# Performance work log

Measured on AMD Instinct MI355X. Metric: run time of the kernel, lower is better.

The kernel has to match this reference:

```python
import jax, jax.numpy as jnp
import numpy as np

N, E, F_IN = 50000, 800000, 64
H, C1, C2 = 4, 32, 64
NUM_GRAPHS, NUM_CLASSES = 128, 8
NEG_SLOPE = 0.2


def _glorot(key, shape):
    fan_in, fan_out = shape[1], shape[0]
    lim = (6.0 / (fan_in + fan_out)) ** 0.5
    return jax.random.uniform(key, shape, jnp.float32, -lim, lim)


def setup_inputs() -> dict:
    key = jax.random.key(0)
    ks = jax.random.split(key, 20)
    x = jax.random.normal(ks[0], (N, F_IN), jnp.float32)
    edge_index = jax.random.randint(ks[1], (2, E), 0, N, jnp.int64)
    batch = jnp.sort(jax.random.randint(ks[2], (N,), 0, NUM_GRAPHS, jnp.int64))
    d1, d2 = H * C1, H * C2
    return {
        "x": x, "edge_index": edge_index, "batch": batch,
        # GATv2 layer 1 (F_IN -> 32, 4 heads)
        "Wl1": _glorot(ks[3], (d1, F_IN)), "bl1": jnp.zeros((d1,), jnp.float32),
        "Wr1": _glorot(ks[4], (d1, F_IN)), "br1": jnp.zeros((d1,), jnp.float32),
        "att1": _glorot(ks[5], (H, C1)), "bias1": jnp.zeros((d1,), jnp.float32),
        # GATv2 layer 2 (128 -> 64, 4 heads)
        "Wl2": _glorot(ks[6], (d2, d1)), "bl2": jnp.zeros((d2,), jnp.float32),
        "Wr2": _glorot(ks[7], (d2, d1)), "br2": jnp.zeros((d2,), jnp.float32),
        "att2": _glorot(ks[8], (H, C2)), "bias2": jnp.zeros((d2,), jnp.float32),
        # classifier: Linear(256,128) -> ReLU -> (Dropout eval=id) -> Linear(128,8)
        "Wf1": _glorot(ks[9], (128, d2)), "bf1": jnp.zeros((128,), jnp.float32),
        "Wf2": _glorot(ks[10], (NUM_CLASSES, 128)), "bf2": jnp.zeros((NUM_CLASSES,), jnp.float32),
    }


def _gatv2(x, src, dst, Wl, bl, Wr, br, att, bias, heads, out_ch):
    # PyG GATv2Conv: xl = lin_l(x) (source), xr = lin_r(x) (target)
    xl = (x @ Wl.T + bl).reshape(N, heads, out_ch)
    xr = (x @ Wr.T + br).reshape(N, heads, out_ch)
    # per-edge score: att . LeakyReLU(xl[j] + xr[i])  -> [E', H]
    e = jnp.sum(jax.nn.leaky_relu(xl[src] + xr[dst], NEG_SLOPE) * att, axis=-1)
    # destination-grouped softmax (self-loops guarantee every node has an edge)
    emax = jax.ops.segment_max(e, dst, num_segments=N)
    ex = jnp.exp(e - emax[dst])
    denom = jax.ops.segment_sum(ex, dst, num_segments=N)
    alpha = ex / denom[dst]  # [E', H]
    out = jax.ops.segment_sum(alpha[:, :, None] * xl[src], dst, num_segments=N)
    return out.reshape(N, heads * out_ch) + bias


def reference(x, edge_index, batch, Wl1, bl1, Wr1, br1, att1, bias1,
              Wl2, bl2, Wr2, br2, att2, bias2, Wf1, bf1, Wf2, bf2):
    # add self loops (PyG default add_self_loops=True)
    loops = jnp.arange(N, dtype=edge_index.dtype)
    src = jnp.concatenate([edge_index[0], loops])
    dst = jnp.concatenate([edge_index[1], loops])
    h = jax.nn.elu(_gatv2(x, src, dst, Wl1, bl1, Wr1, br1, att1, bias1, H, C1))
    h = jax.nn.elu(_gatv2(h, src, dst, Wl2, bl2, Wr2, br2, att2, bias2, H, C2))
    # global mean pool over graphs
    sums = jax.ops.segment_sum(h, batch, num_segments=NUM_GRAPHS)
    cnts = jax.ops.segment_sum(jnp.ones((N,), h.dtype), batch, num_segments=NUM_GRAPHS)
    pooled = sums / jnp.maximum(cnts, 1.0)[:, None]  # [G, 256]
    # classifier (dropout inactive at inference)
    z = jax.nn.relu(pooled @ Wf1.T + bf1)
    return z @ Wf2.T + bf2
```

## Files before the change

kernel.cpp:

```cpp
#include <hip/hip_runtime.h>
#include <hip/hip_bf16.h>
#include <math.h>

#define NN 50000
#define NE 800000
#define NEP (NE + NN)
#define NG 128
#define PSPLIT 16
#define NSB ((NN + 255) / 256)

typedef unsigned short u16;
typedef __bf16 bf16x8 __attribute__((ext_vector_type(8)));
typedef float f32x4 __attribute__((ext_vector_type(4)));

#define L2E 1.4426950408889634f

__device__ __forceinline__ float eluf(float v) {
  return v > 0.0f ? v : expm1f(v);
}
__device__ __forceinline__ float bflo(unsigned u) {
  union { unsigned i; float f; } c; c.i = u << 16; return c.f;
}
__device__ __forceinline__ float bfhi(unsigned u) {
  union { unsigned i; float f; } c; c.i = u & 0xffff0000u; return c.f;
}
__device__ __forceinline__ bf16x8 load8(const u16* p) {
  union { uint4 u; bf16x8 v; } c;
  c.u = *(const uint4*)p;
  return c.v;
}

__global__ __launch_bounds__(256) void k_deg(const int* __restrict__ ei, int* __restrict__ deg) {
  int t = blockIdx.x * 256 + threadIdx.x;
  if (t >= NEP) return;
  int dst = (t < NE) ? ei[NE + t] : (t - NE);
  atomicAdd(&deg[dst], 1);
}

__global__ __launch_bounds__(256) void k_scan1(const int* __restrict__ deg, int* __restrict__ bsum) {
  __shared__ int red[256];
  int i = blockIdx.x * 256 + threadIdx.x;
  red[threadIdx.x] = (i < NN) ? deg[i] : 0;
  __syncthreads();
  for (int off = 128; off > 0; off >>= 1) {
    if (threadIdx.x < off) red[threadIdx.x] += red[threadIdx.x + off];
    __syncthreads();
  }
  if (threadIdx.x == 0) bsum[blockIdx.x] = red[0];
}

__global__ __launch_bounds__(256) void k_scan2(int* __restrict__ bsum) {
  __shared__ int s[256];
  int t = threadIdx.x;
  s[t] = (t < NSB) ? bsum[t] : 0;
  __syncthreads();
  for (int off = 1; off < 256; off <<= 1) {
    int v = (t >= off) ? s[t - off] : 0;
    __syncthreads();
    s[t] += v;
    __syncthreads();
  }
  if (t < NSB) bsum[t] = (t == 0) ? 0 : s[t - 1];
}

__global__ __launch_bounds__(256) void k_scan3(const int* __restrict__ deg, const int* __restrict__ bsum,
                                               int* __restrict__ rowptr) {
  __shared__ int s[256];
  int t = threadIdx.x;
  int i = blockIdx.x * 256 + t;
  s[t] = (i < NN) ? deg[i] : 0;
  __syncthreads();
  for (int off = 1; off < 256; off <<= 1) {
    int v = (t >= off) ? s[t - off] : 0;
    __syncthreads();
    s[t] += v;
    __syncthreads();
  }
  int excl = (t == 0) ? 0 : s[t - 1];
  if (i <= NN) rowptr[i] = bsum[blockIdx.x] + excl;
}

__global__ __launch_bounds__(256) void k_scatter(const int* __restrict__ ei, const int* __restrict__ rowptr,
                                                 int* __restrict__ fill, int* __restrict__ srcidx) {
  int t = blockIdx.x * 256 + threadIdx.x;
  if (t >= NEP) return;
  int src, dst;
  if (t < NE) { src = ei[t]; dst = ei[NE + t]; } else { src = t - NE; dst = src; }
  int pos = atomicAdd(&fill[dst], 1);
  srcidx[rowptr[dst] + pos] = src;
}

__global__ __launch_bounds__(256) void k_cvtx(const float* __restrict__ x, u16* __restrict__ o, int n4) {
  int t = blockIdx.x * 256 + threadIdx.x;
  if (t >= n4) return;
  float4 v = ((const float4*)x)[t];
  __hip_bfloat16 b[4] = {__float2bfloat16(v.x), __float2bfloat16(v.y),
                         __float2bfloat16(v.z), __float2bfloat16(v.w)};
  ((uint2*)o)[t] = *(uint2*)b;
}

__global__ __launch_bounds__(256) void k_cvtw(const float* __restrict__ w1, const float* __restrict__ w2,
                                              const float* __restrict__ w3, const float* __restrict__ w4,
                                              u16* __restrict__ o) {
  int t = blockIdx.x * 256 + threadIdx.x;
  if (t >= 81920) return;
  float v;
  if (t < 8192) v = w1[t];
  else if (t < 16384) v = w2[t - 8192];
  else if (t < 49152) v = w3[t - 16384];
  else v = w4[t - 49152];
  __hip_bfloat16 b = __float2bfloat16(v);
  o[t] = *(u16*)&b;
}

template <int K>
__global__ __launch_bounds__(256) void k_mfma(const u16* __restrict__ Xb,
                                              const u16* __restrict__ Wlb, const u16* __restrict__ Wrb,
                                              const float* __restrict__ bl, const float* __restrict__ br,
                                              __hip_bfloat16* __restrict__ Yl, float* __restrict__ Yr,
                                              int dout) {
  int lane = threadIdx.x & 63;
  int wid = threadIdx.x >> 6;
  int r0 = blockIdx.x * 64 + wid * 16;
  int c0 = blockIdx.y * 64;
  bool isR = (blockIdx.z != 0);
  const u16* W = isR ? Wrb : Wlb;
  const float* bias = isR ? br : bl;

  int arow = min(r0 + (lane & 15), NN - 1);
  int koff = (lane >> 4) * 8;
  const u16* ap = Xb + (size_t)arow * K + koff;
  const u16* bp = W + (size_t)(c0 + (lane & 15)) * K + koff;

  f32x4 acc[4] = {};
#pragma unroll
  for (int ks = 0; ks < K / 32; ++ks) {
    bf16x8 a  = load8(ap + ks * 32);
    bf16x8 b0 = load8(bp + ks * 32);
    bf16x8 b1 = load8(bp + 16 * K + ks * 32);
    bf16x8 b2 = load8(bp + 32 * K + ks * 32);
    bf16x8 b3 = load8(bp + 48 * K + ks * 32);
    acc[0] = __builtin_amdgcn_mfma_f32_16x16x32_bf16(a, b0, acc[0], 0, 0, 0);
    acc[1] = __builtin_amdgcn_mfma_f32_16x16x32_bf16(a, b1, acc[1], 0, 0, 0);
    acc[2] = __builtin_amdgcn_mfma_f32_16x16x32_bf16(a, b2, acc[2], 0, 0, 0);
    acc[3] = __builtin_amdgcn_mfma_f32_16x16x32_bf16(a, b3, acc[3], 0, 0, 0);
  }

  int orow = r0 + ((lane >> 4) << 2);
  int ocol = c0 + (lane & 15);
#pragma unroll
  for (int t = 0; t < 4; ++t) {
    int col = ocol + t * 16;
    float bv = bias[col];
    if (!isR) {
#pragma unroll
      for (int v = 0; v < 4; ++v) {
        int row = orow + v;
        if (row < NN) Yl[(size_t)row * dout + col] = __float2bfloat16(acc[t][v] + bv);
      }
    } else {
#pragma unroll
      for (int v = 0; v < 4; ++v) {
        int row = orow + v;
        if (row < NN) Yr[(size_t)row * dout + col] = acc[t][v] + bv;
      }
    }
  }
}

template <int D, bool OBF16>
__global__ __launch_bounds__(256) void k_fused(const int* __restrict__ rowptr, const int* __restrict__ srcidx,
                                               const u16* __restrict__ xl, const float* __restrict__ xr,
                                               const float* __restrict__ att, const float* __restrict__ bias,
                                               void* __restrict__ outv) {
  constexpr int V = D / 64;
  int lane = threadIdx.x & 63;
  int node = blockIdx.x * 4 + (threadIdx.x >> 6);
  if (node >= NN) return;
  int lo = rowptr[node], hi = rowptr[node + 1];

  float xrv[V], attv[V];
  float rlin = 0.f;
#pragma unroll
  for (int q = 0; q < V; ++q) {
    attv[q] = att[lane * V + q] * (0.4f * L2E);
    xrv[q]  = xr[(size_t)node * D + lane * V + q];
    rlin = fmaf(attv[q], xrv[q], rlin);
  }
#pragma unroll
  for (int off = 1; off < 16; off <<= 1) rlin += __shfl_xor(rlin, off);
  float S0 = 1.5f * rlin;

  const unsigned* xt1 = (const unsigned*)xl;
  const uint2*    xt2 = (const uint2*)xl;

  float denom = 0.f;
  float acc[V] = {};

  auto gather = [&](int j, float* xv) {
    if constexpr (V == 2) {
      unsigned u = xt1[(size_t)j * (D / 2) + lane];
      xv[0] = bflo(u); xv[1] = bfhi(u);
    } else {
      uint2 u = xt2[(size_t)j * (D / 4) + lane];
      xv[0] = bflo(u.x); xv[1] = bfhi(u.x);
      xv[2] = bflo(u.y); xv[3] = bfhi(u.y);
    }
  };
  auto score2 = [&](const float* xv) {
    float pa = 0.f, pl = 0.f;
#pragma unroll
    for (int q = 0; q < V; ++q) {
      float u = xv[q] + xrv[q];
      pa = fmaf(attv[q], fabsf(u), pa);
      pl = fmaf(attv[q], xv[q], pl);
    }
    return fmaf(pl, 1.5f, pa);
  };
  auto update = [&](float p, const float* xv) {
    float w = exp2f(p + S0);
    denom += w;
#pragma unroll
    for (int q = 0; q < V; ++q) acc[q] = fmaf(w, xv[q], acc[q]);
  };

  int s = lo;
  for (; s + 3 < hi; s += 4) {
    int j0 = srcidx[s], j1 = srcidx[s + 1], j2 = srcidx[s + 2], j3 = srcidx[s + 3];
    float xv0[V], xv1[V], xv2[V], xv3[V];
    gather(j0, xv0); gather(j1, xv1); gather(j2, xv2); gather(j3, xv3);
    float p0 = score2(xv0);
    float p1 = score2(xv1);
    float p2 = score2(xv2);
    float p3 = score2(xv3);
#pragma unroll
    for (int off = 1; off < 16; off <<= 1) {
      p0 += __shfl_xor(p0, off);
      p1 += __shfl_xor(p1, off);
      p2 += __shfl_xor(p2, off);
      p3 += __shfl_xor(p3, off);
    }
    update(p0, xv0); update(p1, xv1); update(p2, xv2); update(p3, xv3);
  }
  for (; s < hi; ++s) {
    int j0 = srcidx[s];
    float xv0[V];
    gather(j0, xv0);
    float p0 = score2(xv0);
#pragma unroll
    for (int off = 1; off < 16; off <<= 1) p0 += __shfl_xor(p0, off);
    update(p0, xv0);
  }

  float rd = 1.0f / denom;
  float vals[V];
#pragma unroll
  for (int q = 0; q < V; ++q) vals[q] = eluf(fmaf(acc[q], rd, bias[lane * V + q]));

  if constexpr (OBF16) {
    __hip_bfloat16 tmp[V];
#pragma unroll
    for (int q = 0; q < V; ++q) tmp[q] = __float2bfloat16(vals[q]);
    if constexpr (V == 2) ((unsigned*)outv)[(size_t)node * (D / 2) + lane] = *(unsigned*)tmp;
    else                  ((uint2*)outv)[(size_t)node * (D / 4) + lane] = *(uint2*)tmp;
  } else {
    if constexpr (V == 2) {
      float2 f = {vals[0], vals[1]};
      ((float2*)outv)[(size_t)node * (D / 2) + lane] = f;
    } else {
      float4 f = {vals[0], vals[1], vals[2], vals[3]};
      ((float4*)outv)[(size_t)node * (D / 4) + lane] = f;
    }
  }
}

__device__ __forceinline__ int lowerb(const int* __restrict__ a, int n, int v) {
  int lo = 0, hi = n;
  while (lo < hi) { int mid = (lo + hi) >> 1; if (a[mid] < v) lo = mid + 1; else hi = mid; }
  return lo;
}

__global__ __launch_bounds__(256) void k_pool(const float* __restrict__ h2, const int* __restrict__ batch,
                                              float* __restrict__ pooled_p) {
  int g = blockIdx.x, sp = blockIdx.y, t = threadIdx.x;
  __shared__ int sh[2];
  if (t < 2) sh[t] = lowerb(batch, NN, g + t);
  __syncthreads();
  int lo = sh[0], hi = sh[1];
  int cnt = hi - lo;
  int chunk = (cnt + PSPLIT - 1) / PSPLIT;
  int b = lo + sp * chunk;
  int e = min(b + chunk, hi);
  float acc = 0.f;
  for (int n = b; n < e; ++n) acc += h2[(size_t)n * 256 + t];
  pooled_p[((size_t)g * PSPLIT + sp) * 256 + t] = acc;
}

__global__ __launch_bounds__(128) void k_cls(const float* __restrict__ pooled_p, const int* __restrict__ batch,
                                             const float* __restrict__ Wf1, const float* __restrict__ bf1,
                                             const float* __restrict__ Wf2, const float* __restrict__ bf2,
                                             float* __restrict__ out) {
  __shared__ float p[256];
  __shared__ float z[128];
  __shared__ int sh[2];
  int g = blockIdx.x, t = threadIdx.x;
  if (t < 2) sh[t] = lowerb(batch, NN, g + t);
  __syncthreads();
  float cnt = (float)(sh[1] - sh[0]);
  float rinv = 1.0f / fmaxf(cnt, 1.0f);
  const float* pp = pooled_p + (size_t)g * PSPLIT * 256;
#pragma unroll 1
  for (int c = t; c < 256; c += 128) {
    float s = 0.f;
#pragma unroll
    for (int sp = 0; sp < PSPLIT; ++sp) s += pp[sp * 256 + c];
    p[c] = s * rinv;
  }
  __syncthreads();
  float a = bf1[t];
  const float* wr = Wf1 + (size_t)t * 256;
  for (int k = 0; k < 256; ++k) a += p[k] * wr[k];
  z[t] = fmaxf(a, 0.f);
  __syncthreads();
  if (t < 8) {
    float o = bf2[t];
    const float* w2 = Wf2 + t * 128;
    for (int k = 0; k < 128; ++k) o += z[k] * w2[k];
    out[g * 8 + t] = o;
  }
}

extern "C" void kernel_launch(void* const* d_in, const int* in_sizes, int n_in,
                              void* d_out, int out_size, void* d_ws, size_t ws_size,
                              hipStream_t stream) {
  const float* x     = (const float*)d_in[0];
  const int*   ei    = (const int*)d_in[1];
  const int*   batch = (const int*)d_in[2];
  const float* Wl1 = (const float*)d_in[3];
  const float* bl1 = (const float*)d_in[4];
  const float* Wr1 = (const float*)d_in[5];
  const float* br1 = (const float*)d_in[6];
  const float* att1  = (const float*)d_in[7];
  const float* bias1 = (const float*)d_in[8];
  const float* Wl2 = (const float*)d_in[9];
  const float* bl2 = (const float*)d_in[10];
  const float* Wr2 = (const float*)d_in[11];
  const float* br2 = (const float*)d_in[12];
  const float* att2  = (const float*)d_in[13];
  const float* bias2 = (const float*)d_in[14];
  const float* Wf1 = (const float*)d_in[15];
  const float* bf1 = (const float*)d_in[16];
  const float* Wf2 = (const float*)d_in[17];
  const float* bf2 = (const float*)d_in[18];
  float* out = (float*)d_out;

  char* w = (char*)d_ws;
  size_t off = 0;
  auto alloc = [&](size_t bytes) -> void* {
    void* p = w + off;
    off += (bytes + 255) & ~(size_t)255;
    return p;
  };
  int* rowptr = (int*)alloc((NN + 1) * sizeof(int));
  int* deg    = (int*)alloc(NN * sizeof(int));
  int* fill   = (int*)alloc(NN * sizeof(int));
  int* bsum   = (int*)alloc(NSB * sizeof(int));
  int* srcidx = (int*)alloc((size_t)NEP * sizeof(int));
  u16* Xb1    = (u16*)alloc((size_t)NN * 64 * sizeof(u16));
  u16* Wb     = (u16*)alloc((size_t)81920 * sizeof(u16));
  u16* Wl1b = Wb, *Wr1b = Wb + 8192, *Wl2b = Wb + 16384, *Wr2b = Wb + 49152;
  char* regA  = (char*)alloc((size_t)NN * 128 * 2 + (size_t)NN * 128 * 4);
  __hip_bfloat16* xl1 = (__hip_bfloat16*)regA;
  float*          xr1 = (float*)(regA + (size_t)NN * 128 * 2);
  __hip_bfloat16* xl2 = (__hip_bfloat16*)regA;
  u16*   h1b    = (u16*)alloc((size_t)NN * 128 * sizeof(u16));
  float* xr2    = (float*)alloc((size_t)NN * 256 * sizeof(float));
  float* h2     = xr2;
  float* pooled_p = (float*)alloc((size_t)NG * PSPLIT * 256 * sizeof(float));
  (void)ws_size; (void)in_sizes; (void)n_in; (void)out_size;

  hipMemsetAsync(deg, 0, NN * sizeof(int), stream);
  hipMemsetAsync(fill, 0, NN * sizeof(int), stream);

  const int EB = (NEP + 255) / 256;
  k_deg<<<EB, 256, 0, stream>>>(ei, deg);
  k_scan1<<<NSB, 256, 0, stream>>>(deg, bsum);
  k_scan2<<<1, 256, 0, stream>>>(bsum);
  k_scan3<<<NSB, 256, 0, stream>>>(deg, bsum, rowptr);
  k_scatter<<<EB, 256, 0, stream>>>(ei, rowptr, fill, srcidx);

  k_cvtx<<<(NN * 64 / 4 + 255) / 256, 256, 0, stream>>>(x, Xb1, NN * 64 / 4);
  k_cvtw<<<(81920 + 255) / 256, 256, 0, stream>>>(Wl1, Wr1, Wl2, Wr2, Wb);

  const int RB = (NN + 63) / 64;
  dim3 g1(RB, 2, 2);
  k_mfma<64><<<g1, 256, 0, stream>>>(Xb1, Wl1b, Wr1b, bl1, br1, xl1, xr1, 128);
  k_fused<128, true><<<(NN + 3) / 4, 256, 0, stream>>>(rowptr, srcidx, (const u16*)xl1, xr1,
                                                       att1, bias1, h1b);

  dim3 g2(RB, 4, 2);
  k_mfma<128><<<g2, 256, 0, stream>>>(h1b, Wl2b, Wr2b, bl2, br2, xl2, xr2, 256);
  k_fused<256, false><<<(NN + 3) / 4, 256, 0, stream>>>(rowptr, srcidx, (const u16*)xl2, xr2,
                                                        att2, bias2, h2);

  dim3 gp(NG, PSPLIT);
  k_pool<<<gp, 256, 0, stream>>>(h2, batch, pooled_p);
  k_cls<<<NG, 128, 0, stream>>>(pooled_p, batch, Wf1, bf1, Wf2, bf2, out);
}
```

Before: 349.7 us.

## Fuse x bf16 conversion into MFMA, reuse degree counters, vectorize edge-index loads

Drops the separate x-to-bf16 kernel and converts fp32 rows to bf16 inside the first MFMA GEMM. Reuses the degree array as the scatter fill counter via atomicSub, which removes one memset and one buffer. In the attention kernel it merges the two score accumulators into one FMA chain, uses the hardware exp2 intrinsic, and aligns the edge loop so four source indices load as a single int4. The cost is that the first GEMM now reads fp32 A operands twice (once per column-block and L/R side) and the scatter order within each row is reversed.

```diff
diff --git a/kernel.cpp b/kernel.cpp
--- a/kernel.cpp
+++ b/kernel.cpp
@@ -81,22 +81,13 @@
 }
 
 __global__ __launch_bounds__(256) void k_scatter(const int* __restrict__ ei, const int* __restrict__ rowptr,
-                                                 int* __restrict__ fill, int* __restrict__ srcidx) {
+                                                 int* __restrict__ deg, int* __restrict__ srcidx) {
   int t = blockIdx.x * 256 + threadIdx.x;
   if (t >= NEP) return;
   int src, dst;
   if (t < NE) { src = ei[t]; dst = ei[NE + t]; } else { src = t - NE; dst = src; }
-  int pos = atomicAdd(&fill[dst], 1);
+  int pos = atomicSub(&deg[dst], 1) - 1;
   srcidx[rowptr[dst] + pos] = src;
-}
-
-__global__ __launch_bounds__(256) void k_cvtx(const float* __restrict__ x, u16* __restrict__ o, int n4) {
-  int t = blockIdx.x * 256 + threadIdx.x;
-  if (t >= n4) return;
-  float4 v = ((const float4*)x)[t];
-  __hip_bfloat16 b[4] = {__float2bfloat16(v.x), __float2bfloat16(v.y),
-                         __float2bfloat16(v.z), __float2bfloat16(v.w)};
-  ((uint2*)o)[t] = *(uint2*)b;
 }
 
 __global__ __launch_bounds__(256) void k_cvtw(const float* __restrict__ w1, const float* __restrict__ w2,
@@ -113,8 +104,8 @@
   o[t] = *(u16*)&b;
 }
 
-template <int K>
-__global__ __launch_bounds__(256) void k_mfma(const u16* __restrict__ Xb,
+template <int K, bool AF32>
+__global__ __launch_bounds__(256) void k_mfma(const void* __restrict__ Xin,
                                               const u16* __restrict__ Wlb, const u16* __restrict__ Wrb,
                                               const float* __restrict__ bl, const float* __restrict__ br,
                                               __hip_bfloat16* __restrict__ Yl, float* __restrict__ Yr,
@@ -129,13 +120,22 @@
 
   int arow = min(r0 + (lane & 15), NN - 1);
   int koff = (lane >> 4) * 8;
-  const u16* ap = Xb + (size_t)arow * K + koff;
+  const u16*   aph = (const u16*)Xin + (size_t)arow * K + koff;
+  const float* apf = (const float*)Xin + (size_t)arow * K + koff;
   const u16* bp = W + (size_t)(c0 + (lane & 15)) * K + koff;
 
   f32x4 acc[4] = {};
 #pragma unroll
   for (int ks = 0; ks < K / 32; ++ks) {
-    bf16x8 a  = load8(ap + ks * 32);
+    bf16x8 a;
+    if constexpr (AF32) {
+      float4 f0 = ((const float4*)(apf + ks * 32))[0];
+      float4 f1 = ((const float4*)(apf + ks * 32))[1];
+      a[0] = (__bf16)f0.x; a[1] = (__bf16)f0.y; a[2] = (__bf16)f0.z; a[3] = (__bf16)f0.w;
+      a[4] = (__bf16)f1.x; a[5] = (__bf16)f1.y; a[6] = (__bf16)f1.z; a[7] = (__bf16)f1.w;
+    } else {
+      a = load8(aph + ks * 32);
+    }
     bf16x8 b0 = load8(bp + ks * 32);
     bf16x8 b1 = load8(bp + 16 * K + ks * 32);
     bf16x8 b2 = load8(bp + 32 * K + ks * 32);
@@ -207,32 +207,43 @@
       xv[2] = bflo(u.y); xv[3] = bfhi(u.y);
     }
   };
-  auto score2 = [&](const float* xv) {
-    float pa = 0.f, pl = 0.f;
+  auto score1 = [&](const float* xv) {
+    float p = 0.f;
 #pragma unroll
     for (int q = 0; q < V; ++q) {
       float u = xv[q] + xrv[q];
-      pa = fmaf(attv[q], fabsf(u), pa);
-      pl = fmaf(attv[q], xv[q], pl);
-    }
-    return fmaf(pl, 1.5f, pa);
+      float t = fmaf(1.5f, xv[q], fabsf(u));
+      p = fmaf(attv[q], t, p);
+    }
+    return p;
   };
   auto update = [&](float p, const float* xv) {
-    float w = exp2f(p + S0);
+    float w = __builtin_amdgcn_exp2f(p + S0);
     denom += w;
 #pragma unroll
     for (int q = 0; q < V; ++q) acc[q] = fmaf(w, xv[q], acc[q]);
   };
+  auto single = [&](int s) {
+    int j0 = srcidx[s];
+    float xv0[V];
+    gather(j0, xv0);
+    float p0 = score1(xv0);
+#pragma unroll
+    for (int off = 1; off < 16; off <<= 1) p0 += __shfl_xor(p0, off);
+    update(p0, xv0);
+  };
 
   int s = lo;
+  int pre = min((4 - (lo & 3)) & 3, hi - lo);
+  for (int k = 0; k < pre; ++k, ++s) single(s);
   for (; s + 3 < hi; s += 4) {
-    int j0 = srcidx[s], j1 = srcidx[s + 1], j2 = srcidx[s + 2], j3 = srcidx[s + 3];
+    int4 j4 = *(const int4*)(srcidx + s);
     float xv0[V], xv1[V], xv2[V], xv3[V];
-    gather(j0, xv0); gather(j1, xv1); gather(j2, xv2); gather(j3, xv3);
-    float p0 = score2(xv0);
-    float p1 = score2(xv1);
-    float p2 = score2(xv2);
-    float p3 = score2(xv3);
+    gather(j4.x, xv0); gather(j4.y, xv1); gather(j4.z, xv2); gather(j4.w, xv3);
+    float p0 = score1(xv0);
+    float p1 = score1(xv1);
+    float p2 = score1(xv2);
+    float p3 = score1(xv3);
 #pragma unroll
     for (int off = 1; off < 16; off <<= 1) {
       p0 += __shfl_xor(p0, off);
@@ -242,15 +253,7 @@
     }
     update(p0, xv0); update(p1, xv1); update(p2, xv2); update(p3, xv3);
   }
-  for (; s < hi; ++s) {
-    int j0 = srcidx[s];
-    float xv0[V];
-    gather(j0, xv0);
-    float p0 = score2(xv0);
-#pragma unroll
-    for (int off = 1; off < 16; off <<= 1) p0 += __shfl_xor(p0, off);
-    update(p0, xv0);
-  }
+  for (; s < hi; ++s) single(s);
 
   float rd = 1.0f / denom;
   float vals[V];
@@ -363,10 +366,8 @@
   };
   int* rowptr = (int*)alloc((NN + 1) * sizeof(int));
   int* deg    = (int*)alloc(NN * sizeof(int));
-  int* fill   = (int*)alloc(NN * sizeof(int));
   int* bsum   = (int*)alloc(NSB * sizeof(int));
   int* srcidx = (int*)alloc((size_t)NEP * sizeof(int));
-  u16* Xb1    = (u16*)alloc((size_t)NN * 64 * sizeof(u16));
   u16* Wb     = (u16*)alloc((size_t)81920 * sizeof(u16));
   u16* Wl1b = Wb, *Wr1b = Wb + 8192, *Wl2b = Wb + 16384, *Wr2b = Wb + 49152;
   char* regA  = (char*)alloc((size_t)NN * 128 * 2 + (size_t)NN * 128 * 4);
@@ -380,26 +381,24 @@
   (void)ws_size; (void)in_sizes; (void)n_in; (void)out_size;
 
   hipMemsetAsync(deg, 0, NN * sizeof(int), stream);
-  hipMemsetAsync(fill, 0, NN * sizeof(int), stream);
 
   const int EB = (NEP + 255) / 256;
   k_deg<<<EB, 256, 0, stream>>>(ei, deg);
   k_scan1<<<NSB, 256, 0, stream>>>(deg, bsum);
   k_scan2<<<1, 256, 0, stream>>>(bsum);
   k_scan3<<<NSB, 256, 0, stream>>>(deg, bsum, rowptr);
-  k_scatter<<<EB, 256, 0, stream>>>(ei, rowptr, fill, srcidx);
-
-  k_cvtx<<<(NN * 64 / 4 + 255) / 256, 256, 0, stream>>>(x, Xb1, NN * 64 / 4);
+  k_scatter<<<EB, 256, 0, stream>>>(ei, rowptr, deg, srcidx);
+
   k_cvtw<<<(81920 + 255) / 256, 256, 0, stream>>>(Wl1, Wr1, Wl2, Wr2, Wb);
 
   const int RB = (NN + 63) / 64;
   dim3 g1(RB, 2, 2);
-  k_mfma<64><<<g1, 256, 0, stream>>>(Xb1, Wl1b, Wr1b, bl1, br1, xl1, xr1, 128);
+  k_mfma<64, true><<<g1, 256, 0, stream>>>(x, Wl1b, Wr1b, bl1, br1, xl1, xr1, 128);
   k_fused<128, true><<<(NN + 3) / 4, 256, 0, stream>>>(rowptr, srcidx, (const u16*)xl1, xr1,
                                                        att1, bias1, h1b);
 
   dim3 g2(RB, 4, 2);
-  k_mfma<128><<<g2, 256, 0, stream>>>(h1b, Wl2b, Wr2b, bl2, br2, xl2, xr2, 256);
+  k_mfma<128, false><<<g2, 256, 0, stream>>>(h1b, Wl2b, Wr2b, bl2, br2, xl2, xr2, 256);
   k_fused<256, false><<<(NN + 3) / 4, 256, 0, stream>>>(rowptr, srcidx, (const u16*)xl2, xr2,
                                                         att2, bias2, h2);
 
```

New measurement: 360.7 us. 1.03x slower.
